# Kernel tuning notes

Measured on AMD Instinct MI355X. Metric: run time of the kernel, lower is better.

Reference implementation:

```python
import jax, jax.numpy as jnp
import numpy as np

B, S, D, H = 2, 2048, 1024, 16
HD = D // H  # 64


def setup_inputs() -> dict:
    key = jax.random.key(0)
    ks = jax.random.split(key, 10)
    q = jax.random.normal(ks[0], (B, S, D), dtype=jnp.float32)
    k = jax.random.normal(ks[1], (B, S, D), dtype=jnp.float32)
    v = jax.random.normal(ks[2], (B, S, D), dtype=jnp.float32)
    # additive mask: 1 where attention is disallowed (causal), broadcast over B,H
    mask = (1.0 - jnp.tril(jnp.ones((S, S), dtype=jnp.float32)))[None, None, :, :]
    sc = 1.0 / np.sqrt(D)
    Wk = jax.random.normal(ks[3], (D, D), dtype=jnp.float32) * sc
    bk = jnp.zeros((D,), dtype=jnp.float32)
    Wv = jax.random.normal(ks[4], (D, D), dtype=jnp.float32) * sc
    bv = jnp.zeros((D,), dtype=jnp.float32)
    Wo = jax.random.normal(ks[5], (D, D), dtype=jnp.float32) * sc
    bo = jnp.zeros((D,), dtype=jnp.float32)
    return {"q": q, "k": k, "v": v, "mask": mask,
            "Wk": Wk, "bk": bk, "Wv": Wv, "bv": bv, "Wo": Wo, "bo": bo}


def _split_heads(x):
    b, s, d = x.shape
    return x.reshape(b, s, H, HD).transpose(0, 2, 1, 3)  # [B,H,S,HD]


def reference(q, k, v, mask, Wk, bk, Wv, bv, Wo, bo):
    # NOTE: source bug reproduced — q is projected with Wk (wq is unused).
    _q = _split_heads(q @ Wk + bk)
    _k = _split_heads(k @ Wk + bk)
    _v = _split_heads(v @ Wv + bv)
    scale = jnp.sqrt(jnp.float32(HD)) + 1e-8
    score = jnp.einsum('bhqd,bhkd->bhqk', _q, _k) / scale
    score = score + mask * (-1e9)
    attn = jax.nn.softmax(score, axis=-1)
    o = jnp.einsum('bhqk,bhkd->bhqd', attn, _v)
    o = o.transpose(0, 2, 1, 3).reshape(q.shape[0], q.shape[1], -1)  # [B,S,D]
    # dropout is identity at inference (training=False)
    return o @ Wo + bo
```

## Files before the change

kernel.cpp:

```cpp
#include <hip/hip_runtime.h>


#define Bn 2
#define Sn 2048
#define Dn 1024
#define Hn 16
#define HDn 64

typedef short bs8 __attribute__((ext_vector_type(8)));
typedef float f32x4 __attribute__((ext_vector_type(4)));
typedef float f32x16 __attribute__((ext_vector_type(16)));
typedef unsigned int u32;
typedef unsigned int u32x2 __attribute__((ext_vector_type(2)));
typedef unsigned int u32x4 __attribute__((ext_vector_type(4)));

__device__ __forceinline__ short f2bf(float f) {
    u32 x = __builtin_bit_cast(u32, f);
    x = x + 0x7fffu + ((x >> 16) & 1u);
    return (short)(x >> 16);
}
__device__ __forceinline__ u32 cvtpk(float lo, float hi) {
    u32 r;
    asm("v_cvt_pk_bf16_f32 %0, %1, %2" : "=v"(r) : "v"(lo), "v"(hi));
    return r;
}
__device__ __forceinline__ u32x2 pl32swap(u32 a, u32 b) {
    return __builtin_amdgcn_permlane32_swap(a, b, false, false);
}
__device__ __forceinline__ float asf(u32 x) { return __builtin_bit_cast(float, x); }
__device__ __forceinline__ u32 asu(float x) { return __builtin_bit_cast(u32, x); }
__device__ __forceinline__ void gload16(const void* g, void* l) {
    __builtin_amdgcn_global_load_lds(
        (const __attribute__((address_space(1))) u32*)g,
        (__attribute__((address_space(3))) u32*)l, 16, 0, 0);
}

__global__ __launch_bounds__(256) void cvt_qkv(const float* __restrict__ q,
                                               const float* __restrict__ k,
                                               const float* __restrict__ v,
                                               short* __restrict__ out) {
    int z = blockIdx.y;
    const float* in = z == 0 ? q : z == 1 ? k : v;
    short* o = out + (size_t)z * (Bn * Sn * Dn);
    int i = blockIdx.x * 256 + threadIdx.x;
    const f32x4* p = reinterpret_cast<const f32x4*>(in) + (size_t)i * 2;
    f32x4 a = p[0], b = p[1];
    bs8 ov;
    ov[0]=f2bf(a[0]); ov[1]=f2bf(a[1]); ov[2]=f2bf(a[2]); ov[3]=f2bf(a[3]);
    ov[4]=f2bf(b[0]); ov[5]=f2bf(b[1]); ov[6]=f2bf(b[2]); ov[7]=f2bf(b[3]);
    reinterpret_cast<bs8*>(o)[i] = ov;
}

__global__ __launch_bounds__(256) void cvt_w(const float* __restrict__ Wk,
                                             const float* __restrict__ Wv,
                                             const float* __restrict__ Wo,
                                             short* __restrict__ Wt) {
    __shared__ float tile[32][33];
    int z = blockIdx.z;
    const float* W = z == 0 ? Wk : z == 1 ? Wv : Wo;
    short* o = Wt + (size_t)z * Dn * Dn;
    int tx = threadIdx.x & 31;
    int ty = threadIdx.x >> 5;
    int bi = blockIdx.y * 32;
    int bo = blockIdx.x * 32;
    #pragma unroll
    for (int k2 = 0; k2 < 4; k2++)
        tile[ty + k2*8][tx] = W[(size_t)(bi + ty + k2*8) * Dn + bo + tx];
    __syncthreads();
    #pragma unroll
    for (int k2 = 0; k2 < 4; k2++)
        o[(size_t)(bo + ty + k2*8) * Dn + bi + tx] = f2bf(tile[tx][ty + k2*8]);
}

__global__ __launch_bounds__(256) void proj3(const short* __restrict__ qb,
                                             const short* __restrict__ kb,
                                             const short* __restrict__ vb,
                                             const short* __restrict__ Wall,
                                             const float* __restrict__ bk,
                                             const float* __restrict__ bv,
                                             short* __restrict__ Qp,
                                             short* __restrict__ Kp,
                                             short* __restrict__ Vtp) {
    constexpr int K = Dn;
    __shared__ __align__(16) short As[128 * 32];
    __shared__ __align__(16) short Bs[128 * 32];
    int z = blockIdx.z;
    const short* A  = z == 0 ? qb : z == 1 ? kb : vb;
    const short* Bt = z == 2 ? Wall + (1 << 20) : Wall;
    const float* bias = z == 2 ? bv : bk;
    int tid = threadIdx.x;
    int m0 = blockIdx.x * 128, n0 = blockIdx.y * 128;
    int w = tid >> 6, lane = tid & 63;
    int wr = (w >> 1) * 64, wc = (w & 1) * 64;
    int fr = lane & 15, fq = lane >> 4;
    f32x4 acc[4][4] = {};
    const short* Ag  = A  + (size_t)(m0 + (tid >> 2)) * K + (tid & 3) * 8;
    const short* Ag2 = Ag + (size_t)64 * K;
    const short* Bg  = Bt + (size_t)(n0 + (tid >> 2)) * K + (tid & 3) * 8;
    const short* Bg2 = Bg + (size_t)64 * K;
    short* AsL = As + tid * 8;
    short* BsL = Bs + tid * 8;

    for (int k0 = 0; k0 < K; k0 += 32) {
        gload16(Ag + k0, AsL);
        gload16(Ag2 + k0, AsL + 2048);
        gload16(Bg + k0, BsL);
        gload16(Bg2 + k0, BsL + 2048);
        __syncthreads();
        bs8 af[4], bfv[4];
        #pragma unroll
        for (int i = 0; i < 4; i++)
            af[i] = *reinterpret_cast<const bs8*>(&As[(wr + i*16 + fr) * 32 + fq * 8]);
        #pragma unroll
        for (int j = 0; j < 4; j++)
            bfv[j] = *reinterpret_cast<const bs8*>(&Bs[(wc + j*16 + fr) * 32 + fq * 8]);
        #pragma unroll
        for (int i = 0; i < 4; i++)
            #pragma unroll
            for (int j = 0; j < 4; j++)
                acc[i][j] = __builtin_amdgcn_mfma_f32_16x16x32_bf16(af[i], bfv[j], acc[i][j], 0, 0, 0);
        __syncthreads();
    }

    if (z == 2) {
        #pragma unroll
        for (int j = 0; j < 4; j++) {
            int col = n0 + wc + j*16 + fr;
            float bvv = bias[col];
            #pragma unroll
            for (int i = 0; i < 4; i++) {
                int row0 = m0 + wr + i*16 + fq*4;
                int bb = row0 >> 11, s0 = row0 & (Sn - 1);
                size_t base = (size_t)bb * (Dn * Sn) + (size_t)col * Sn + s0;
                u32x2 pv;
                pv[0] = cvtpk(acc[i][j][0] + bvv, acc[i][j][1] + bvv);
                pv[1] = cvtpk(acc[i][j][2] + bvv, acc[i][j][3] + bvv);
                *reinterpret_cast<u32x2*>(&Vtp[base]) = pv;
            }
        }
    } else {
        float sc = (z == 0) ? 0.18033688011112042f : 1.0f;
        short* outp = (z == 0) ? Qp : Kp;
        #pragma unroll
        for (int j = 0; j < 4; j++) {
            int col = n0 + wc + j*16 + fr;
            float bvv = bias[col];
            #pragma unroll
            for (int i = 0; i < 4; i++) {
                int row0 = m0 + wr + i*16 + fq*4;
                #pragma unroll
                for (int r = 0; r < 4; r++)
                    outp[(size_t)(row0 + r) * Dn + col] = f2bf((acc[i][j][r] + bvv) * sc);
            }
        }
    }
}

__global__ __launch_bounds__(256) void gemm_out(const short* __restrict__ A,
                                                const short* __restrict__ Bt,
                                                const float* __restrict__ bias,
                                                float* __restrict__ Cout) {
    constexpr int K = Dn, N = Dn;
    __shared__ __align__(16) short As[64][32];
    __shared__ __align__(16) short Bs[128][32];
    int tid = threadIdx.x;
    int m0 = blockIdx.x * 64, n0 = blockIdx.y * 128;
    int w = tid >> 6, lane = tid & 63;
    int wr = (w >> 1) * 32, wc = (w & 1) * 64;
    int fr = lane & 15, fq = lane >> 4;
    f32x4 acc[2][4] = {};
    const short* Ag  = A  + (size_t)(m0 + (tid >> 2)) * K + (tid & 3) * 8;
    const short* Bg0 = Bt + (size_t)(n0 + (tid >> 2)) * K + (tid & 3) * 8;
    const short* Bg1 = Bg0 + (size_t)64 * K;
    short* AsL  = &As[0][0] + tid * 8;
    short* BsL0 = &Bs[0][0] + tid * 8;
    short* BsL1 = BsL0 + 2048;

    for (int k0 = 0; k0 < K; k0 += 32) {
        gload16(Ag + k0, AsL);
        gload16(Bg0 + k0, BsL0);
        gload16(Bg1 + k0, BsL1);
        __syncthreads();
        bs8 af[2], bfv[4];
        #pragma unroll
        for (int i = 0; i < 2; i++)
            af[i] = *reinterpret_cast<const bs8*>(&As[wr + i*16 + fr][fq*8]);
        #pragma unroll
        for (int j = 0; j < 4; j++)
            bfv[j] = *reinterpret_cast<const bs8*>(&Bs[wc + j*16 + fr][fq*8]);
        #pragma unroll
        for (int i = 0; i < 2; i++)
            #pragma unroll
            for (int j = 0; j < 4; j++)
                acc[i][j] = __builtin_amdgcn_mfma_f32_16x16x32_bf16(af[i], bfv[j], acc[i][j], 0, 0, 0);
        __syncthreads();
    }
    #pragma unroll
    for (int j = 0; j < 4; j++) {
        int col = n0 + wc + j*16 + fr;
        float bv = bias[col];
        #pragma unroll
        for (int i = 0; i < 2; i++) {
            int row0 = m0 + wr + i*16 + fq*4;
            #pragma unroll
            for (int r = 0; r < 4; r++)
                Cout[(size_t)(row0 + r) * N + col] = acc[i][j][r] + bv;
        }
    }
}

__global__ __launch_bounds__(256) void attn_fwd(const short* __restrict__ Qp,
                                                const short* __restrict__ Kp,
                                                const short* __restrict__ Vt,
                                                short* __restrict__ O) {
    __shared__ __align__(16) char Kb[64 * 128];
    __shared__ __align__(16) char Vb[64 * 128];
    __shared__ __align__(16) u32 Ot[4][32 * 36];
    int qt = 15 - (int)blockIdx.x;
    int bh = blockIdx.y, bb = bh >> 4, h = bh & 15;
    int tid = threadIdx.x, w = tid >> 6, lane = tid & 63;
    int lq = lane & 31, hi = lane >> 5;
    int q0 = qt * 128 + w * 32;
    int qg = q0 + lq;
    int qw_end = q0 + 31;

    const short* Qrow = Qp + (size_t)(bb * Sn + qg) * Dn + h * HDn;
    bs8 qf[4];
    #pragma unroll
    for (int t = 0; t < 4; t++)
        qf[t] = *reinterpret_cast<const bs8*>(Qrow + 16 * t + 8 * hi);

    f32x16 oacc0 = {}, oacc1 = {};
    float m_run = -3e38f, l_run = 0.f;

    int srow = 16 * w + (lane >> 3);
    int scol = (8 * (lane & 7)) ^ ((lane >> 3) << 3);
    const short* KgB = Kp + (size_t)(bb * Sn + srow) * Dn + h * HDn + scol;
    const short* VgB = Vt + (size_t)bb * (Dn * Sn) + (size_t)(h * HDn + srow) * Sn + scol;
    char* KdA = Kb + (16 * w) * 128;
    char* KdB = KdA + 8 * 128;
    char* VdA = Vb + (16 * w) * 128;
    char* VdB = VdA + 8 * 128;

    int rsw = (lq & 7) << 4;
    const char* Krow0 = Kb + lq * 128;
    const char* Krow1 = Kb + (32 + lq) * 128;
    const char* Vrow0 = Vb + lq * 128;
    const char* Vrow1 = Vb + (32 + lq) * 128;

    int nkv = 2 * qt + 2;
    for (int kt = 0; kt < nkv; kt++) {
        int kv0 = kt * 64;
        __syncthreads();
        gload16(KgB + (size_t)kv0 * Dn, KdA);
        gload16(KgB + (size_t)kv0 * Dn + 8 * Dn, KdB);
        gload16(VgB + kv0, VdA);
        gload16(VgB + kv0 + 8 * Sn, VdB);
        __syncthreads();
        if (kv0 > qw_end) continue;

        f32x16 s0 = {}, s1 = {};
        #pragma unroll
        for (int t = 0; t < 4; t++) {
            int ofs = (32 * t + 16 * hi) ^ rsw;
            bs8 kf0 = *reinterpret_cast<const bs8*>(Krow0 + ofs);
            bs8 kf1 = *reinterpret_cast<const bs8*>(Krow1 + ofs);
            s0 = __builtin_amdgcn_mfma_f32_32x32x16_bf16(kf0, qf[t], s0, 0, 0, 0);
            s1 = __builtin_amdgcn_mfma_f32_32x32x16_bf16(kf1, qf[t], s1, 0, 0, 0);
        }
        if (kv0 + 63 > q0) {
            #pragma unroll
            for (int r = 0; r < 16; r++) {
                int c = (r & 3) + 8 * (r >> 2) + 4 * hi;
                if (kv0 + c > qg)      s0[r] = -1.8e8f;
                if (kv0 + 32 + c > qg) s1[r] = -1.8e8f;
            }
        }

        float mloc = fmaxf(s0[0], s1[0]);
        #pragma unroll
        for (int r = 1; r < 16; r++) mloc = fmaxf(mloc, fmaxf(s0[r], s1[r]));
        {
            u32x2 rr = pl32swap(asu(mloc), asu(mloc));
            mloc = fmaxf(asf(rr[0]), asf(rr[1]));
        }
        if (!__all(mloc <= m_run + 8.0f)) {
            float mn = fmaxf(m_run, mloc);
            float fac = exp2f(m_run - mn);
            m_run = mn; l_run *= fac;
            oacc0 *= fac; oacc1 *= fac;
        }
        float ss = 0.f;
        #pragma unroll
        for (int r = 0; r < 16; r++) {
            s0[r] = exp2f(s0[r] - m_run); ss += s0[r];
            s1[r] = exp2f(s1[r] - m_run); ss += s1[r];
        }
        l_run += ss;

        u32 W0[8], W1[8];
        #pragma unroll
        for (int u = 0; u < 8; u++) {
            W0[u] = cvtpk(s0[2*u], s0[2*u+1]);
            W1[u] = cvtpk(s1[2*u], s1[2*u+1]);
        }
        u32x4 Bf[4];
        #pragma unroll
        for (int t = 0; t < 4; t++) {
            int u0 = 4 * (t & 1);
            u32 a0 = (t < 2) ? W0[u0]     : W1[u0];
            u32 b0 = (t < 2) ? W0[u0 + 2] : W1[u0 + 2];
            u32 a1 = (t < 2) ? W0[u0 + 1] : W1[u0 + 1];
            u32 b1 = (t < 2) ? W0[u0 + 3] : W1[u0 + 3];
            u32x2 r0 = pl32swap(a0, b0);
            u32x2 r1 = pl32swap(a1, b1);
            Bf[t][0] = r0[0]; Bf[t][1] = r1[0]; Bf[t][2] = r0[1]; Bf[t][3] = r1[1];
        }

        #pragma unroll
        for (int t = 0; t < 4; t++) {
            bs8 pB = __builtin_bit_cast(bs8, Bf[t]);
            int ofs = (32 * t + 16 * hi) ^ rsw;
            bs8 vf0 = *reinterpret_cast<const bs8*>(Vrow0 + ofs);
            bs8 vf1 = *reinterpret_cast<const bs8*>(Vrow1 + ofs);
            oacc0 = __builtin_amdgcn_mfma_f32_32x32x16_bf16(vf0, pB, oacc0, 0, 0, 0);
            oacc1 = __builtin_amdgcn_mfma_f32_32x32x16_bf16(vf1, pB, oacc1, 0, 0, 0);
        }
    }

    {
        u32x2 rr = pl32swap(asu(l_run), asu(l_run));
        l_run = asf(rr[0]) + asf(rr[1]);
    }
    float inv = 1.f / l_run;

    u32* OtW = Ot[w];
    #pragma unroll
    for (int m = 0; m < 2; m++) {
        f32x16 oo = m ? oacc1 : oacc0;
        #pragma unroll
        for (int u = 0; u < 8; u += 2) {
            u32x2 wv;
            wv[0] = cvtpk(oo[2*u] * inv,     oo[2*u+1] * inv);
            wv[1] = cvtpk(oo[2*u+2] * inv,   oo[2*u+3] * inv);
            int widx = 16 * m + 4 * (u >> 1) + 2 * hi;
            *reinterpret_cast<u32x2*>(OtW + lq * 36 + widx) = wv;
        }
    }
    __builtin_amdgcn_wave_barrier();
    int q2 = lane >> 1, hh = lane & 1;
    const u32* rp = OtW + q2 * 36 + hh * 16;
    short* Og = O + (size_t)(bb * Sn + q0 + q2) * Dn + h * HDn + hh * 32;
    #pragma unroll
    for (int c = 0; c < 4; c++) {
        u32x4 vv = *reinterpret_cast<const u32x4*>(rp + 4 * c);
        *reinterpret_cast<u32x4*>(Og + 8 * c) = vv;
    }
}

extern "C" void kernel_launch(void* const* d_in, const int* in_sizes, int n_in,
                              void* d_out, int out_size, void* d_ws, size_t ws_size,
                              hipStream_t stream) {
    const float* q  = (const float*)d_in[0];
    const float* k  = (const float*)d_in[1];
    const float* v  = (const float*)d_in[2];
    const float* Wk = (const float*)d_in[4];
    const float* bk = (const float*)d_in[5];
    const float* Wv = (const float*)d_in[6];
    const float* bv = (const float*)d_in[7];
    const float* Wo = (const float*)d_in[8];
    const float* bo = (const float*)d_in[9];

    char* ws = (char*)d_ws;
    const size_t MB = (size_t)1 << 20;
    short* Wall = (short*)ws;
    short* Wot  = Wall + 2 * (1 << 20);
    short* qb   = (short*)(ws + 6*MB);
    short* kb   = (short*)(ws + 14*MB);
    short* vb   = (short*)(ws + 22*MB);
    short* Qp   = (short*)(ws + 30*MB);
    short* Kp   = (short*)(ws + 38*MB);
    short* Vtp  = (short*)(ws + 46*MB);
    short* Oa   = qb;

    cvt_qkv<<<dim3(2048, 3), dim3(256), 0, stream>>>(q, k, v, qb);
    cvt_w<<<dim3(32, 32, 3), dim3(256), 0, stream>>>(Wk, Wv, Wo, Wall);

    proj3<<<dim3(32, 8, 3), dim3(256), 0, stream>>>(qb, kb, vb, Wall, bk, bv, Qp, Kp, Vtp);

    attn_fwd<<<dim3(16, 32), dim3(256), 0, stream>>>(Qp, Kp, Vtp, Oa);

    gemm_out<<<dim3(64, 8), dim3(256), 0, stream>>>(Oa, Wot, bo, (float*)d_out);
}
```

Measured before the change: 262.4 us.

## Double-buffer GEMM LDS tiles and rewrite attention as single-wave blocks

Both projection GEMMs now double-buffer their LDS tiles, issuing the next k-slice load before computing the current one, which drops one barrier per iteration. The attention kernel becomes one-wave blocks of 32 queries that read K and V fragments straight from global memory without LDS staging. It skips the upper 32-key half on the diagonal tile and uses a swizzled block order. This trades LDS reuse across waves for finer-grained causal work and fewer barriers, but it increases global and L2 traffic for K and V.

After: 299.4 us. 14.1% more time.

```diff
diff --git a/kernel.cpp b/kernel.cpp
--- a/kernel.cpp
+++ b/kernel.cpp
@@ -82,8 +82,8 @@
                                              short* __restrict__ Kp,
                                              short* __restrict__ Vtp) {
     constexpr int K = Dn;
-    __shared__ __align__(16) short As[128 * 32];
-    __shared__ __align__(16) short Bs[128 * 32];
+    __shared__ __align__(16) short As[2][128 * 32];
+    __shared__ __align__(16) short Bs[2][128 * 32];
     int z = blockIdx.z;
     const short* A  = z == 0 ? qb : z == 1 ? kb : vb;
     const short* Bt = z == 2 ? Wall + (1 << 20) : Wall;
@@ -98,28 +98,37 @@
     const short* Ag2 = Ag + (size_t)64 * K;
     const short* Bg  = Bt + (size_t)(n0 + (tid >> 2)) * K + (tid & 3) * 8;
     const short* Bg2 = Bg + (size_t)64 * K;
-    short* AsL = As + tid * 8;
-    short* BsL = Bs + tid * 8;
-
+    short* AsL = &As[0][0] + tid * 8;
+    short* BsL = &Bs[0][0] + tid * 8;
+
+    auto STAGE = [&](int buf, int k0) {
+        gload16(Ag  + k0, AsL + buf * 4096);
+        gload16(Ag2 + k0, AsL + buf * 4096 + 2048);
+        gload16(Bg  + k0, BsL + buf * 4096);
+        gload16(Bg2 + k0, BsL + buf * 4096 + 2048);
+    };
+
+    STAGE(0, 0);
+    __syncthreads();
+    int cur = 0;
     for (int k0 = 0; k0 < K; k0 += 32) {
-        gload16(Ag + k0, AsL);
-        gload16(Ag2 + k0, AsL + 2048);
-        gload16(Bg + k0, BsL);
-        gload16(Bg2 + k0, BsL + 2048);
-        __syncthreads();
+        if (k0 + 32 < K) STAGE(cur ^ 1, k0 + 32);
+        const short* Asb = &As[cur][0];
+        const short* Bsb = &Bs[cur][0];
         bs8 af[4], bfv[4];
         #pragma unroll
         for (int i = 0; i < 4; i++)
-            af[i] = *reinterpret_cast<const bs8*>(&As[(wr + i*16 + fr) * 32 + fq * 8]);
+            af[i] = *reinterpret_cast<const bs8*>(&Asb[(wr + i*16 + fr) * 32 + fq * 8]);
         #pragma unroll
         for (int j = 0; j < 4; j++)
-            bfv[j] = *reinterpret_cast<const bs8*>(&Bs[(wc + j*16 + fr) * 32 + fq * 8]);
+            bfv[j] = *reinterpret_cast<const bs8*>(&Bsb[(wc + j*16 + fr) * 32 + fq * 8]);
         #pragma unroll
         for (int i = 0; i < 4; i++)
             #pragma unroll
             for (int j = 0; j < 4; j++)
                 acc[i][j] = __builtin_amdgcn_mfma_f32_16x16x32_bf16(af[i], bfv[j], acc[i][j], 0, 0, 0);
         __syncthreads();
+        cur ^= 1;
     }
 
     if (z == 2) {
@@ -161,8 +170,8 @@
                                                 const float* __restrict__ bias,
                                                 float* __restrict__ Cout) {
     constexpr int K = Dn, N = Dn;
-    __shared__ __align__(16) short As[64][32];
-    __shared__ __align__(16) short Bs[128][32];
+    __shared__ __align__(16) short As[2][64 * 32];
+    __shared__ __align__(16) short Bs[2][128 * 32];
     int tid = threadIdx.x;
     int m0 = blockIdx.x * 64, n0 = blockIdx.y * 128;
     int w = tid >> 6, lane = tid & 63;
@@ -172,28 +181,36 @@
     const short* Ag  = A  + (size_t)(m0 + (tid >> 2)) * K + (tid & 3) * 8;
     const short* Bg0 = Bt + (size_t)(n0 + (tid >> 2)) * K + (tid & 3) * 8;
     const short* Bg1 = Bg0 + (size_t)64 * K;
-    short* AsL  = &As[0][0] + tid * 8;
-    short* BsL0 = &Bs[0][0] + tid * 8;
-    short* BsL1 = BsL0 + 2048;
-
+    short* AsL = &As[0][0] + tid * 8;
+    short* BsL = &Bs[0][0] + tid * 8;
+
+    auto STAGE = [&](int buf, int k0) {
+        gload16(Ag  + k0, AsL + buf * 2048);
+        gload16(Bg0 + k0, BsL + buf * 4096);
+        gload16(Bg1 + k0, BsL + buf * 4096 + 2048);
+    };
+
+    STAGE(0, 0);
+    __syncthreads();
+    int cur = 0;
     for (int k0 = 0; k0 < K; k0 += 32) {
-        gload16(Ag + k0, AsL);
-        gload16(Bg0 + k0, BsL0);
-        gload16(Bg1 + k0, BsL1);
-        __syncthreads();
+        if (k0 + 32 < K) STAGE(cur ^ 1, k0 + 32);
+        const short* Asb = &As[cur][0];
+        const short* Bsb = &Bs[cur][0];
         bs8 af[2], bfv[4];
         #pragma unroll
         for (int i = 0; i < 2; i++)
-            af[i] = *reinterpret_cast<const bs8*>(&As[wr + i*16 + fr][fq*8]);
+            af[i] = *reinterpret_cast<const bs8*>(&Asb[(wr + i*16 + fr) * 32 + fq * 8]);
         #pragma unroll
         for (int j = 0; j < 4; j++)
-            bfv[j] = *reinterpret_cast<const bs8*>(&Bs[wc + j*16 + fr][fq*8]);
+            bfv[j] = *reinterpret_cast<const bs8*>(&Bsb[(wc + j*16 + fr) * 32 + fq * 8]);
         #pragma unroll
         for (int i = 0; i < 2; i++)
             #pragma unroll
             for (int j = 0; j < 4; j++)
                 acc[i][j] = __builtin_amdgcn_mfma_f32_16x16x32_bf16(af[i], bfv[j], acc[i][j], 0, 0, 0);
         __syncthreads();
+        cur ^= 1;
     }
     #pragma unroll
     for (int j = 0; j < 4; j++) {
@@ -209,77 +226,76 @@
     }
 }
 
-__global__ __launch_bounds__(256) void attn_fwd(const short* __restrict__ Qp,
-                                                const short* __restrict__ Kp,
-                                                const short* __restrict__ Vt,
-                                                short* __restrict__ O) {
-    __shared__ __align__(16) char Kb[64 * 128];
-    __shared__ __align__(16) char Vb[64 * 128];
-    __shared__ __align__(16) u32 Ot[4][32 * 36];
-    int qt = 15 - (int)blockIdx.x;
-    int bh = blockIdx.y, bb = bh >> 4, h = bh & 15;
-    int tid = threadIdx.x, w = tid >> 6, lane = tid & 63;
+__global__ __launch_bounds__(64) void attn_fwd(const short* __restrict__ Qp,
+                                               const short* __restrict__ Kp,
+                                               const short* __restrict__ Vt,
+                                               short* __restrict__ O) {
+    __shared__ __align__(16) u32 Ot[32 * 36];
+    int bid = blockIdx.x;
+    int swz = (bid & 7) * 256 + (bid >> 3);
+    int bh = swz >> 6;
+    int j  = 63 - (swz & 63);
+    int bb = bh >> 4, h = bh & 15;
+    int lane = threadIdx.x;
     int lq = lane & 31, hi = lane >> 5;
-    int q0 = qt * 128 + w * 32;
+    int q0 = j * 32;
     int qg = q0 + lq;
-    int qw_end = q0 + 31;
-
-    const short* Qrow = Qp + (size_t)(bb * Sn + qg) * Dn + h * HDn;
+
+    const short* Qrow = Qp + (size_t)(bb * Sn + qg) * Dn + h * HDn + 8 * hi;
     bs8 qf[4];
     #pragma unroll
     for (int t = 0; t < 4; t++)
-        qf[t] = *reinterpret_cast<const bs8*>(Qrow + 16 * t + 8 * hi);
+        qf[t] = *reinterpret_cast<const bs8*>(Qrow + 16 * t);
+
+    const short* Kb0 = Kp + (size_t)(bb * Sn + lq) * Dn + h * HDn + 8 * hi;
+    const short* Vb0 = Vt + (size_t)bb * (Dn * Sn) + (size_t)(h * HDn + lq) * Sn + 8 * hi;
 
     f32x16 oacc0 = {}, oacc1 = {};
     float m_run = -3e38f, l_run = 0.f;
 
-    int srow = 16 * w + (lane >> 3);
-    int scol = (8 * (lane & 7)) ^ ((lane >> 3) << 3);
-    const short* KgB = Kp + (size_t)(bb * Sn + srow) * Dn + h * HDn + scol;
-    const short* VgB = Vt + (size_t)bb * (Dn * Sn) + (size_t)(h * HDn + srow) * Sn + scol;
-    char* KdA = Kb + (16 * w) * 128;
-    char* KdB = KdA + 8 * 128;
-    char* VdA = Vb + (16 * w) * 128;
-    char* VdB = VdA + 8 * 128;
-
-    int rsw = (lq & 7) << 4;
-    const char* Krow0 = Kb + lq * 128;
-    const char* Krow1 = Kb + (32 + lq) * 128;
-    const char* Vrow0 = Vb + lq * 128;
-    const char* Vrow1 = Vb + (32 + lq) * 128;
-
-    int nkv = 2 * qt + 2;
+    int nkv = (j >> 1) + 1;
     for (int kt = 0; kt < nkv; kt++) {
         int kv0 = kt * 64;
-        __syncthreads();
-        gload16(KgB + (size_t)kv0 * Dn, KdA);
-        gload16(KgB + (size_t)kv0 * Dn + 8 * Dn, KdB);
-        gload16(VgB + kv0, VdA);
-        gload16(VgB + kv0 + 8 * Sn, VdB);
-        __syncthreads();
-        if (kv0 > qw_end) continue;
+        bool dia = (kt == nkv - 1);
+        bool s1live = (kv0 + 32 <= q0 + 31);
+        const short* Kt = Kb0 + (size_t)kv0 * Dn;
+        const short* Vtt = Vb0 + kv0;
+
+        bs8 kf0[4], kf1[4];
+        #pragma unroll
+        for (int t = 0; t < 4; t++)
+            kf0[t] = *reinterpret_cast<const bs8*>(Kt + 16 * t);
+        if (s1live) {
+            #pragma unroll
+            for (int t = 0; t < 4; t++)
+                kf1[t] = *reinterpret_cast<const bs8*>(Kt + (size_t)32 * Dn + 16 * t);
+        }
 
         f32x16 s0 = {}, s1 = {};
         #pragma unroll
-        for (int t = 0; t < 4; t++) {
-            int ofs = (32 * t + 16 * hi) ^ rsw;
-            bs8 kf0 = *reinterpret_cast<const bs8*>(Krow0 + ofs);
-            bs8 kf1 = *reinterpret_cast<const bs8*>(Krow1 + ofs);
-            s0 = __builtin_amdgcn_mfma_f32_32x32x16_bf16(kf0, qf[t], s0, 0, 0, 0);
-            s1 = __builtin_amdgcn_mfma_f32_32x32x16_bf16(kf1, qf[t], s1, 0, 0, 0);
-        }
-        if (kv0 + 63 > q0) {
+        for (int t = 0; t < 4; t++)
+            s0 = __builtin_amdgcn_mfma_f32_32x32x16_bf16(kf0[t], qf[t], s0, 0, 0, 0);
+        if (s1live) {
+            #pragma unroll
+            for (int t = 0; t < 4; t++)
+                s1 = __builtin_amdgcn_mfma_f32_32x32x16_bf16(kf1[t], qf[t], s1, 0, 0, 0);
+        }
+        if (dia) {
             #pragma unroll
             for (int r = 0; r < 16; r++) {
                 int c = (r & 3) + 8 * (r >> 2) + 4 * hi;
-                if (kv0 + c > qg)      s0[r] = -1.8e8f;
-                if (kv0 + 32 + c > qg) s1[r] = -1.8e8f;
+                if (kv0 + c > qg) s0[r] = -1.8e8f;
+                if (s1live && kv0 + 32 + c > qg) s1[r] = -1.8e8f;
             }
         }
 
-        float mloc = fmaxf(s0[0], s1[0]);
-        #pragma unroll
-        for (int r = 1; r < 16; r++) mloc = fmaxf(mloc, fmaxf(s0[r], s1[r]));
+        float mloc = s0[0];
+        #pragma unroll
+        for (int r = 1; r < 16; r++) mloc = fmaxf(mloc, s0[r]);
+        if (s1live) {
+            #pragma unroll
+            for (int r = 0; r < 16; r++) mloc = fmaxf(mloc, s1[r]);
+        }
         {
             u32x2 rr = pl32swap(asu(mloc), asu(mloc));
             mloc = fmaxf(asf(rr[0]), asf(rr[1]));
@@ -292,39 +308,45 @@
         }
         float ss = 0.f;
         #pragma unroll
-        for (int r = 0; r < 16; r++) {
-            s0[r] = exp2f(s0[r] - m_run); ss += s0[r];
-            s1[r] = exp2f(s1[r] - m_run); ss += s1[r];
+        for (int r = 0; r < 16; r++) { s0[r] = exp2f(s0[r] - m_run); ss += s0[r]; }
+        if (s1live) {
+            #pragma unroll
+            for (int r = 0; r < 16; r++) { s1[r] = exp2f(s1[r] - m_run); ss += s1[r]; }
         }
         l_run += ss;
 
         u32 W0[8], W1[8];
         #pragma unroll
-        for (int u = 0; u < 8; u++) {
-            W0[u] = cvtpk(s0[2*u], s0[2*u+1]);
-            W1[u] = cvtpk(s1[2*u], s1[2*u+1]);
-        }
-        u32x4 Bf[4];
-        #pragma unroll
-        for (int t = 0; t < 4; t++) {
-            int u0 = 4 * (t & 1);
-            u32 a0 = (t < 2) ? W0[u0]     : W1[u0];
-            u32 b0 = (t < 2) ? W0[u0 + 2] : W1[u0 + 2];
-            u32 a1 = (t < 2) ? W0[u0 + 1] : W1[u0 + 1];
-            u32 b1 = (t < 2) ? W0[u0 + 3] : W1[u0 + 3];
-            u32x2 r0 = pl32swap(a0, b0);
-            u32x2 r1 = pl32swap(a1, b1);
-            Bf[t][0] = r0[0]; Bf[t][1] = r1[0]; Bf[t][2] = r0[1]; Bf[t][3] = r1[1];
-        }
-
-        #pragma unroll
-        for (int t = 0; t < 4; t++) {
-            bs8 pB = __builtin_bit_cast(bs8, Bf[t]);
-            int ofs = (32 * t + 16 * hi) ^ rsw;
-            bs8 vf0 = *reinterpret_cast<const bs8*>(Vrow0 + ofs);
-            bs8 vf1 = *reinterpret_cast<const bs8*>(Vrow1 + ofs);
+        for (int u = 0; u < 8; u++) W0[u] = cvtpk(s0[2*u], s0[2*u+1]);
+        if (s1live) {
+            #pragma unroll
+            for (int u = 0; u < 8; u++) W1[u] = cvtpk(s1[2*u], s1[2*u+1]);
+        }
+        #pragma unroll
+        for (int t = 0; t < 2; t++) {
+            int u0 = 4 * t;
+            u32x2 r0 = pl32swap(W0[u0],     W0[u0 + 2]);
+            u32x2 r1 = pl32swap(W0[u0 + 1], W0[u0 + 3]);
+            u32x4 bf; bf[0] = r0[0]; bf[1] = r1[0]; bf[2] = r0[1]; bf[3] = r1[1];
+            bs8 pB = __builtin_bit_cast(bs8, bf);
+            bs8 vf0 = *reinterpret_cast<const bs8*>(Vtt + 16 * t);
+            bs8 vf1 = *reinterpret_cast<const bs8*>(Vtt + (size_t)32 * Sn + 16 * t);
             oacc0 = __builtin_amdgcn_mfma_f32_32x32x16_bf16(vf0, pB, oacc0, 0, 0, 0);
             oacc1 = __builtin_amdgcn_mfma_f32_32x32x16_bf16(vf1, pB, oacc1, 0, 0, 0);
+        }
+        if (s1live) {
+            #pragma unroll
+            for (int t = 2; t < 4; t++) {
+                int u0 = 4 * (t & 1);
+                u32x2 r0 = pl32swap(W1[u0],     W1[u0 + 2]);
+                u32x2 r1 = pl32swap(W1[u0 + 1], W1[u0 + 3]);
+                u32x4 bf; bf[0] = r0[0]; bf[1] = r1[0]; bf[2] = r0[1]; bf[3] = r1[1];
+                bs8 pB = __builtin_bit_cast(bs8, bf);
+                bs8 vf0 = *reinterpret_cast<const bs8*>(Vtt + 16 * t);
+                bs8 vf1 = *reinterpret_cast<const bs8*>(Vtt + (size_t)32 * Sn + 16 * t);
+                oacc0 = __builtin_amdgcn_mfma_f32_32x32x16_bf16(vf0, pB, oacc0, 0, 0, 0);
+                oacc1 = __builtin_amdgcn_mfma_f32_32x32x16_bf16(vf1, pB, oacc1, 0, 0, 0);
+            }
         }
     }
 
@@ -334,22 +356,21 @@
     }
     float inv = 1.f / l_run;
 
-    u32* OtW = Ot[w];
     #pragma unroll
     for (int m = 0; m < 2; m++) {
         f32x16 oo = m ? oacc1 : oacc0;
         #pragma unroll
         for (int u = 0; u < 8; u += 2) {
             u32x2 wv;
-            wv[0] = cvtpk(oo[2*u] * inv,     oo[2*u+1] * inv);
-            wv[1] = cvtpk(oo[2*u+2] * inv,   oo[2*u+3] * inv);
+            wv[0] = cvtpk(oo[2*u] * inv,   oo[2*u+1] * inv);
+            wv[1] = cvtpk(oo[2*u+2] * inv, oo[2*u+3] * inv);
             int widx = 16 * m + 4 * (u >> 1) + 2 * hi;
-            *reinterpret_cast<u32x2*>(OtW + lq * 36 + widx) = wv;
+            *reinterpret_cast<u32x2*>(Ot + lq * 36 + widx) = wv;
         }
     }
     __builtin_amdgcn_wave_barrier();
     int q2 = lane >> 1, hh = lane & 1;
-    const u32* rp = OtW + q2 * 36 + hh * 16;
+    const u32* rp = Ot + q2 * 36 + hh * 16;
     short* Og = O + (size_t)(bb * Sn + q0 + q2) * Dn + h * HDn + hh * 32;
     #pragma unroll
     for (int c = 0; c < 4; c++) {
@@ -388,7 +409,7 @@
 
     proj3<<<dim3(32, 8, 3), dim3(256), 0, stream>>>(qb, kb, vb, Wall, bk, bv, Qp, Kp, Vtp);
 
-    attn_fwd<<<dim3(16, 32), dim3(256), 0, stream>>>(Qp, Kp, Vtp, Oa);
+    attn_fwd<<<dim3(2048), dim3(64), 0, stream>>>(Qp, Kp, Vtp, Oa);
 
     gemm_out<<<dim3(64, 8), dim3(256), 0, stream>>>(Oa, Wot, bo, (float*)d_out);
 }
```
